# Kernel optimization log

Measured on AMD Instinct MI355X. Metric: run time of the kernel, lower is better.

## Reference

```python
import jax, jax.numpy as jnp
import numpy as np

N, FP, H, E, B = 60000, 120, 512, 3, 600
NNZ = 5_000_000
NFORCE = 3 * N
ELEMENTS = jnp.array([1, 8, 29], dtype=jnp.int32)  # unique_atoms (H, O, Cu)


def setup_inputs():
    key = jax.random.key(0)
    ks = jax.random.split(key, 10)
    fingerprints = jax.random.normal(ks[0], (N, FP), jnp.float32)
    atomic_numbers = ELEMENTS[jax.random.randint(ks[1], (N,), 0, E)]
    image_idx = jnp.sort(jax.random.randint(ks[2], (N,), 0, B)).astype(jnp.int32)
    W1 = jax.random.normal(ks[3], (E, FP, H), jnp.float32) / np.float32(np.sqrt(FP))
    b1 = jnp.zeros((E, H), jnp.float32)
    W2 = jax.random.normal(ks[4], (E, H, H), jnp.float32) / np.float32(np.sqrt(H))
    b2 = jnp.zeros((E, H), jnp.float32)
    W3 = jax.random.normal(ks[5], (E, H, 1), jnp.float32) / np.float32(np.sqrt(H))
    b3 = jnp.zeros((E, 1), jnp.float32)
    # sparse fprimes [N*FP, 3*N] in COO form
    fprime_rows = jax.random.randint(ks[6], (NNZ,), 0, N * FP).astype(jnp.int32)
    fprime_cols = jax.random.randint(ks[7], (NNZ,), 0, NFORCE).astype(jnp.int32)
    fprime_vals = jax.random.normal(ks[8], (NNZ,), jnp.float32) * 0.01
    return {"fingerprints": fingerprints, "atomic_numbers": atomic_numbers,
            "image_idx": image_idx, "W1": W1, "b1": b1, "W2": W2, "b2": b2,
            "W3": W3, "b3": b3, "fprime_rows": fprime_rows,
            "fprime_cols": fprime_cols, "fprime_vals": fprime_vals}


def _energy(fingerprints, W1, b1, W2, b2, W3, b3, mask, image_idx):
    # stacked per-element 3-layer tanh MLPs, evaluated densely over all atoms
    h = jnp.tanh(jnp.einsum('nf,efh->enh', fingerprints, W1) + b1[:, None, :])
    h = jnp.tanh(jnp.einsum('enh,ehk->enk', h, W2) + b2[:, None, :])
    out = jnp.einsum('enh,eho->eno', h, W3) + b3[:, None, :]  # [E, N, 1]
    o = jnp.sum(mask.T * out[..., 0], axis=0)  # mask-select per-atom energy [N]
    return jax.ops.segment_sum(o, image_idx, num_segments=B)  # per-image energy [B]


def reference(fingerprints, atomic_numbers, image_idx, W1, b1, W2, b2, W3, b3,
              fprime_rows, fprime_cols, fprime_vals):
    # ElementMask: one-hot over unique atomic numbers
    mask = (atomic_numbers[:, None] == ELEMENTS[None, :]).astype(fingerprints.dtype)  # [N, E]
    efn = lambda fp: _energy(fp, W1, b1, W2, b2, W3, b3, mask, image_idx)
    energy, vjp_fn = jax.vjp(efn, fingerprints)
    # grad of energy wrt fingerprints with grad_outputs = ones
    g = vjp_fn(jnp.ones_like(energy))[0].reshape(-1)  # [N*FP]
    # forces = -fprimes^T @ g  via sparse scatter
    forces = -jax.ops.segment_sum(fprime_vals * g[fprime_rows], fprime_cols,
                                  num_segments=NFORCE).reshape(-1, 3)  # [N, 3]
    return (energy, forces)
```

## Files before the change

kernel.cpp:

```cpp
#include <hip/hip_runtime.h>

#define N_ATOMS 60000
#define FPD 120
#define HD 512
#define EE 3
#define BB 600
#define NNZ_C 5000000
#define NFORCE (3 * N_ATOMS)
#define TB 32
#define CBITS 12
#define NBUCK ((NFORCE + 4095) / 4096)
#define NSLOT 16

typedef unsigned short ushort_t;
typedef unsigned int uint_t;
typedef unsigned long long u64_t;
typedef __attribute__((ext_vector_type(8))) __bf16 bf16x8;
typedef __attribute__((ext_vector_type(4))) float f32x4;
typedef __attribute__((ext_vector_type(4))) int i32x4;

union BF8 { f32x4 f; bf16x8 h; };

__device__ __forceinline__ ushort_t f2bf(float x) {
    uint_t u = __builtin_bit_cast(uint_t, x);
    u = (u + 0x7FFFu + ((u >> 16) & 1u)) >> 16;
    return (ushort_t)u;
}
__device__ __forceinline__ float bf2f(ushort_t s) {
    uint_t u = ((uint_t)s) << 16;
    return __builtin_bit_cast(float, u);
}
__device__ __forceinline__ float fast_tanh(float x) {
    float e2 = __expf(2.f * x);
    return fmaf(-2.f, __frcp_rn(e2 + 1.f), 1.f);
}

__global__ __launch_bounds__(256) void build_lists(const int* __restrict__ z,
                                                   int* __restrict__ counts,
                                                   int* __restrict__ lists) {
    __shared__ int lc[3];
    __shared__ int lbase[3];
    const int t = threadIdx.x;
    if (t < 3) lc[t] = 0;
    __syncthreads();
    const int i = blockIdx.x * 256 + t;
    int e = 0, pos = 0;
    if (i < N_ATOMS) {
        int zi = z[i];
        e = (zi == 1) ? 0 : ((zi == 8) ? 1 : 2);
        pos = atomicAdd(&lc[e], 1);
    }
    __syncthreads();
    if (t < 3) lbase[t] = atomicAdd(&counts[t], lc[t]);
    __syncthreads();
    if (i < N_ATOMS) lists[e * N_ATOMS + lbase[e] + pos] = i;
}

#define R_W2 (EE * 16 * 32 * 512)
#define R_W1 (EE * 4 * 32 * 512)
#define R_W1T (EE * 16 * 8 * 512)
__global__ __launch_bounds__(256) void pack_all(
    const float* __restrict__ W1, const float* __restrict__ W2,
    ushort_t* __restrict__ W1p, ushort_t* __restrict__ W2p,
    ushort_t* __restrict__ W2Tp, ushort_t* __restrict__ W1Tp) {
    int idx = blockIdx.x * 256 + threadIdx.x;
    if (idx < R_W2) {
        int p = idx;
        int j = p & 7, L = (p >> 3) & 63, ct = (p >> 9) & 31, ks = (p >> 14) & 15, e = p >> 18;
        int k = ks * 32 + ((L >> 4) << 3) + j;
        int n = (ct << 4) + (L & 15);
        W2p[p]  = f2bf(W2[((e << 9) + k) * 512 + n]);
        W2Tp[p] = f2bf(W2[((e << 9) + n) * 512 + k]);
    } else if (idx < R_W2 + R_W1) {
        int p = idx - R_W2;
        int j = p & 7, L = (p >> 3) & 63, ct = (p >> 9) & 31, ks = (p >> 14) & 3, e = p >> 16;
        int k = ks * 32 + ((L >> 4) << 3) + j;
        int n = (ct << 4) + (L & 15);
        W1p[p] = (k < FPD) ? f2bf(W1[(e * FPD + k) * 512 + n]) : (ushort_t)0;
    } else if (idx < R_W2 + R_W1 + R_W1T) {
        int p = idx - R_W2 - R_W1;
        int j = p & 7, L = (p >> 3) & 63, ct = (p >> 9) & 7, ks = (p >> 12) & 15, e = p >> 16;
        int k = ks * 32 + ((L >> 4) << 3) + j;
        int n = (ct << 4) + (L & 15);
        W1Tp[p] = (n < FPD) ? f2bf(W1[(e * FPD + n) * 512 + k]) : (ushort_t)0;
    }
}

#define STR 520
#define FSTR 136

__global__ __launch_bounds__(512, 4) void mlp_mfma(
    const float* __restrict__ fps, const int* __restrict__ image_idx,
    const float* __restrict__ b1, const float* __restrict__ b2,
    const float* __restrict__ W3, const float* __restrict__ b3,
    const ushort_t* __restrict__ W1p, const ushort_t* __restrict__ W2p,
    const ushort_t* __restrict__ W2Tp, const ushort_t* __restrict__ W1Tp,
    const int* __restrict__ counts, const int* __restrict__ lists,
    float* __restrict__ energy, ushort_t* __restrict__ g) {
    __shared__ ushort_t sH1[TB * STR];
    __shared__ ushort_t sD[TB * STR];
    __shared__ float sW3[512];
    __shared__ float eAcc[TB];
    __shared__ int sAtom[TB];
    __shared__ int sImg[TB];

    const int e = blockIdx.x % EE;
    const int tile = blockIdx.x / EE;
    const int cnt = counts[e];
    const int base = tile * TB;
    if (base >= cnt) return;
    const int nA = min(TB, cnt - base);
    const int* lst = lists + e * N_ATOMS + base;

    const int t = threadIdx.x;
    const int w = t >> 6, lane = t & 63, quad = lane >> 4, lc = lane & 15;

    if (t < TB) {
        int a = (t < nA) ? lst[t] : -1;
        sAtom[t] = a;
        sImg[t] = (a >= 0) ? image_idx[a] : 0;
        eAcc[t] = 0.f;
    }
    if (t < 512) sW3[t] = W3[e * 512 + t];
    for (int i = t; i < TB * 128; i += 512) {
        int a = i >> 7, f = i & 127;
        float v = 0.f;
        if (f < FPD && a < nA) v = __builtin_nontemporal_load(&fps[(long long)lst[a] * FPD + f]);
        sD[a * FSTR + f] = f2bf(v);
    }
    __syncthreads();

    float b1c[4], b2c[4];
#pragma unroll
    for (int c = 0; c < 4; c++) {
        int col = w * 64 + c * 16 + lc;
        b1c[c] = b1[e * 512 + col];
        b2c[c] = b2[e * 512 + col];
    }

    f32x4 acc[2][4];

#pragma unroll
    for (int rt = 0; rt < 2; rt++)
#pragma unroll
        for (int c = 0; c < 4; c++) acc[rt][c] = (f32x4)0.f;
    {
        const ushort_t* wbase = W1p + ((size_t)(e * 4) * 32 + w * 4) * 512 + lane * 8;
        BF8 bb[4][4];
#pragma unroll
        for (int ks = 0; ks < 4; ks++)
#pragma unroll
            for (int c = 0; c < 4; c++)
                bb[ks][c].f = *(const f32x4*)(wbase + ((size_t)ks * 32 + c) * 512);
#pragma unroll
        for (int ks = 0; ks < 4; ks++) {
            bf16x8 a0 = *(const bf16x8*)((const char*)sD + lc * (FSTR * 2) + ks * 64 + quad * 16);
            bf16x8 a1 = *(const bf16x8*)((const char*)sD + (16 + lc) * (FSTR * 2) + ks * 64 + quad * 16);
#pragma unroll
            for (int c = 0; c < 4; c++) {
                acc[0][c] = __builtin_amdgcn_mfma_f32_16x16x32_bf16(a0, bb[ks][c].h, acc[0][c], 0, 0, 0);
                acc[1][c] = __builtin_amdgcn_mfma_f32_16x16x32_bf16(a1, bb[ks][c].h, acc[1][c], 0, 0, 0);
            }
        }
    }
#pragma unroll
    for (int c = 0; c < 4; c++) {
        int col = w * 64 + c * 16 + lc;
#pragma unroll
        for (int rt = 0; rt < 2; rt++)
#pragma unroll
            for (int r = 0; r < 4; r++) {
                int row = rt * 16 + quad * 4 + r;
                sH1[row * STR + col] = f2bf(fast_tanh(acc[rt][c][r] + b1c[c]));
            }
    }
    __syncthreads();

#pragma unroll
    for (int rt = 0; rt < 2; rt++)
#pragma unroll
        for (int c = 0; c < 4; c++) acc[rt][c] = (f32x4)0.f;
    {
        const ushort_t* wbase = W2p + ((size_t)(e * 16) * 32 + w * 4) * 512 + lane * 8;
#pragma unroll
        for (int ksc = 0; ksc < 4; ksc++) {
            BF8 bb[4][4];
#pragma unroll
            for (int kk = 0; kk < 4; kk++)
#pragma unroll
                for (int c = 0; c < 4; c++)
                    bb[kk][c].f = *(const f32x4*)(wbase + (size_t)(ksc * 4 + kk) * 32 * 512 + (size_t)c * 512);
#pragma unroll
            for (int kk = 0; kk < 4; kk++) {
                int ks = ksc * 4 + kk;
                bf16x8 a0 = *(const bf16x8*)((const char*)sH1 + lc * (STR * 2) + ks * 64 + quad * 16);
                bf16x8 a1 = *(const bf16x8*)((const char*)sH1 + (16 + lc) * (STR * 2) + ks * 64 + quad * 16);
#pragma unroll
                for (int c = 0; c < 4; c++) {
                    acc[0][c] = __builtin_amdgcn_mfma_f32_16x16x32_bf16(a0, bb[kk][c].h, acc[0][c], 0, 0, 0);
                    acc[1][c] = __builtin_amdgcn_mfma_f32_16x16x32_bf16(a1, bb[kk][c].h, acc[1][c], 0, 0, 0);
                }
            }
        }
    }
    {
        float ep[2][4];
#pragma unroll
        for (int rt = 0; rt < 2; rt++)
#pragma unroll
            for (int r = 0; r < 4; r++) ep[rt][r] = 0.f;
#pragma unroll
        for (int c = 0; c < 4; c++) {
            int col = w * 64 + c * 16 + lc;
            float w3c = sW3[col];
#pragma unroll
            for (int rt = 0; rt < 2; rt++)
#pragma unroll
                for (int r = 0; r < 4; r++) {
                    int row = rt * 16 + quad * 4 + r;
                    float h2 = fast_tanh(acc[rt][c][r] + b2c[c]);
                    ep[rt][r] += h2 * w3c;
                    sD[row * STR + col] = f2bf(w3c * (1.f - h2 * h2));
                }
        }
#pragma unroll
        for (int rt = 0; rt < 2; rt++)
#pragma unroll
            for (int r = 0; r < 4; r++) {
                float p = ep[rt][r];
                p += __shfl_xor(p, 1);
                p += __shfl_xor(p, 2);
                p += __shfl_xor(p, 4);
                p += __shfl_xor(p, 8);
                if (lc == 0) atomicAdd(&eAcc[rt * 16 + quad * 4 + r], p);
            }
    }
    __syncthreads();

    if (t < nA) atomicAdd(&energy[sImg[t]], eAcc[t] + b3[e]);

#pragma unroll
    for (int rt = 0; rt < 2; rt++)
#pragma unroll
        for (int c = 0; c < 4; c++) acc[rt][c] = (f32x4)0.f;
    {
        const ushort_t* wbase = W2Tp + ((size_t)(e * 16) * 32 + w * 4) * 512 + lane * 8;
#pragma unroll
        for (int ksc = 0; ksc < 4; ksc++) {
            BF8 bb[4][4];
#pragma unroll
            for (int kk = 0; kk < 4; kk++)
#pragma unroll
                for (int c = 0; c < 4; c++)
                    bb[kk][c].f = *(const f32x4*)(wbase + (size_t)(ksc * 4 + kk) * 32 * 512 + (size_t)c * 512);
#pragma unroll
            for (int kk = 0; kk < 4; kk++) {
                int ks = ksc * 4 + kk;
                bf16x8 a0 = *(const bf16x8*)((const char*)sD + lc * (STR * 2) + ks * 64 + quad * 16);
                bf16x8 a1 = *(const bf16x8*)((const char*)sD + (16 + lc) * (STR * 2) + ks * 64 + quad * 16);
#pragma unroll
                for (int c = 0; c < 4; c++) {
                    acc[0][c] = __builtin_amdgcn_mfma_f32_16x16x32_bf16(a0, bb[kk][c].h, acc[0][c], 0, 0, 0);
                    acc[1][c] = __builtin_amdgcn_mfma_f32_16x16x32_bf16(a1, bb[kk][c].h, acc[1][c], 0, 0, 0);
                }
            }
        }
    }
#pragma unroll
    for (int c = 0; c < 4; c++) {
        int col = w * 64 + c * 16 + lc;
#pragma unroll
        for (int rt = 0; rt < 2; rt++)
#pragma unroll
            for (int r = 0; r < 4; r++) {
                int row = rt * 16 + quad * 4 + r;
                float h1v = bf2f(sH1[row * STR + col]);
                acc[rt][c][r] *= (1.f - h1v * h1v);
            }
    }
    __syncthreads();
#pragma unroll
    for (int c = 0; c < 4; c++) {
        int col = w * 64 + c * 16 + lc;
#pragma unroll
        for (int rt = 0; rt < 2; rt++)
#pragma unroll
            for (int r = 0; r < 4; r++) {
                int row = rt * 16 + quad * 4 + r;
                sH1[row * STR + col] = f2bf(acc[rt][c][r]);
            }
    }
    __syncthreads();

    f32x4 acc7[2];
#pragma unroll
    for (int rt = 0; rt < 2; rt++) acc7[rt] = (f32x4)0.f;
    {
        const ushort_t* wbase = W1Tp + ((size_t)(e * 16) * 8 + w) * 512 + lane * 8;
#pragma unroll
        for (int ksc = 0; ksc < 2; ksc++) {
            BF8 bb[8];
#pragma unroll
            for (int kk = 0; kk < 8; kk++)
                bb[kk].f = *(const f32x4*)(wbase + (size_t)(ksc * 8 + kk) * 8 * 512);
#pragma unroll
            for (int kk = 0; kk < 8; kk++) {
                int ks = ksc * 8 + kk;
                bf16x8 a0 = *(const bf16x8*)((const char*)sH1 + lc * (STR * 2) + ks * 64 + quad * 16);
                bf16x8 a1 = *(const bf16x8*)((const char*)sH1 + (16 + lc) * (STR * 2) + ks * 64 + quad * 16);
                acc7[0] = __builtin_amdgcn_mfma_f32_16x16x32_bf16(a0, bb[kk].h, acc7[0], 0, 0, 0);
                acc7[1] = __builtin_amdgcn_mfma_f32_16x16x32_bf16(a1, bb[kk].h, acc7[1], 0, 0, 0);
            }
        }
    }
    {
        int col = w * 16 + lc;
#pragma unroll
        for (int rt = 0; rt < 2; rt++)
#pragma unroll
            for (int r = 0; r < 4; r++) {
                int row = rt * 16 + quad * 4 + r;
                if (col < FPD && row < nA)
                    g[(long long)sAtom[row] * FPD + col] = f2bf(acc7[rt][r]);
            }
    }
}

__global__ __launch_bounds__(256) void bucket_hist(const int* __restrict__ cols,
                                                   int* __restrict__ bcnt) {
    __shared__ int h[NBUCK];
    const int t = threadIdx.x;
    if (t < NBUCK) h[t] = 0;
    __syncthreads();
    const int nv = NNZ_C / 4;
    for (int vk = blockIdx.x * 256 + t; vk < nv; vk += gridDim.x * 256) {
        i32x4 c = __builtin_nontemporal_load((const i32x4*)cols + vk);
        atomicAdd(&h[c.x >> CBITS], 1);
        atomicAdd(&h[c.y >> CBITS], 1);
        atomicAdd(&h[c.z >> CBITS], 1);
        atomicAdd(&h[c.w >> CBITS], 1);
    }
    __syncthreads();
    if (t < NBUCK) atomicAdd(&bcnt[t], h[t]);
}

__global__ void bucket_scan(const int* __restrict__ bcnt, int* __restrict__ bbase,
                            int* __restrict__ bcur) {
    if (threadIdx.x == 0 && blockIdx.x == 0) {
        int s = 0;
        for (int i = 0; i < NBUCK; i++) { bbase[i] = s; bcur[i] = s; s += bcnt[i]; }
    }
}

__global__ __launch_bounds__(256) void bucket_scatter(
    const int* __restrict__ rows, const int* __restrict__ cols,
    const float* __restrict__ vals, int* __restrict__ bcur,
    u64_t* __restrict__ bpack) {
    __shared__ int lcnt[NBUCK];
    __shared__ int lcur[NBUCK];
    const int t = threadIdx.x;
    if (t < NBUCK) lcnt[t] = 0;
    __syncthreads();
    const int vk0 = blockIdx.x * 2048;
    i32x4 ccache[8];
    int nb[8][4];
#pragma unroll
    for (int i = 0; i < 8; i++) {
        int vk = vk0 + i * 256 + t;
        if (vk * 4 < NNZ_C) {
            i32x4 c = __builtin_nontemporal_load((const i32x4*)cols + vk);
            ccache[i] = c;
            nb[i][0] = c.x >> CBITS; nb[i][1] = c.y >> CBITS;
            nb[i][2] = c.z >> CBITS; nb[i][3] = c.w >> CBITS;
            atomicAdd(&lcnt[nb[i][0]], 1);
            atomicAdd(&lcnt[nb[i][1]], 1);
            atomicAdd(&lcnt[nb[i][2]], 1);
            atomicAdd(&lcnt[nb[i][3]], 1);
        } else {
            nb[i][0] = -1;
        }
    }
    __syncthreads();
    if (t < NBUCK) lcur[t] = atomicAdd(&bcur[t], lcnt[t]);
    __syncthreads();
#pragma unroll
    for (int i = 0; i < 8; i++) {
        int vk = vk0 + i * 256 + t;
        if (vk * 4 < NNZ_C) {
            i32x4 r = __builtin_nontemporal_load((const i32x4*)rows + vk);
            f32x4 v = __builtin_nontemporal_load((const f32x4*)vals + vk);
            int rr[4] = {r.x, r.y, r.z, r.w};
            int cc[4] = {ccache[i].x, ccache[i].y, ccache[i].z, ccache[i].w};
            float vv[4] = {v.x, v.y, v.z, v.w};
#pragma unroll
            for (int u = 0; u < 4; u++) {
                int pos = atomicAdd(&lcur[nb[i][u]], 1);
                u64_t pk = (u64_t)(uint_t)rr[u] |
                           ((u64_t)(uint_t)(cc[u] & ((1 << CBITS) - 1)) << 23) |
                           ((u64_t)f2bf(vv[u]) << 35);
                bpack[pos] = pk;
            }
        }
    }
}

__global__ __launch_bounds__(256) void scatter_lds(
    const u64_t* __restrict__ bpack, const int* __restrict__ bbase,
    const int* __restrict__ bcnt, const ushort_t* __restrict__ g,
    float* __restrict__ forcesP) {
    __shared__ float facc[1 << CBITS];
    const int b = blockIdx.x >> 4;
    const int s = blockIdx.x & (NSLOT - 1);
    const int t = threadIdx.x;
    for (int i = t; i < (1 << CBITS); i += 256) facc[i] = 0.f;
    __syncthreads();
    const int base = bbase[b];
    const int end = base + bcnt[b];
    for (int i = base + s * 256 + t; i < end; i += NSLOT * 256) {
        u64_t pk = bpack[i];
        int r = (int)(pk & 0x7FFFFFu);
        int cin = (int)((pk >> 23) & 0xFFFu);
        float v = bf2f((ushort_t)(pk >> 35));
        atomicAdd(&facc[cin], -v * bf2f(g[r]));
    }
    __syncthreads();
    const int colbase = b << CBITS;
    float* fp = forcesP + (size_t)s * NFORCE;
    for (int i = t; i < (1 << CBITS); i += 256) {
        int col = colbase + i;
        if (col < NFORCE) __builtin_nontemporal_store(facc[i], &fp[col]);
    }
}

__global__ void reduce_forces(const float* __restrict__ forcesP, float* __restrict__ forces) {
    int i = blockIdx.x * blockDim.x + threadIdx.x;
    if (i >= NFORCE) return;
    float s = 0.f;
#pragma unroll
    for (int x = 0; x < NSLOT; x++) s += forcesP[(size_t)x * NFORCE + i];
    forces[i] = s;
}

__global__ __launch_bounds__(256) void scatter_forces(
    const int* __restrict__ rows, const int* __restrict__ cols,
    const float* __restrict__ vals, const ushort_t* __restrict__ g,
    float* __restrict__ forcesP) {
    int k = blockIdx.x * 256 + threadIdx.x;
    if (k >= NNZ_C / 4) return;
    int slot = blockIdx.x & (NSLOT - 1);
    i32x4 r = __builtin_nontemporal_load((const i32x4*)rows + k);
    i32x4 c = __builtin_nontemporal_load((const i32x4*)cols + k);
    f32x4 v = __builtin_nontemporal_load((const f32x4*)vals + k);
    float* fp = forcesP + (size_t)slot * NFORCE;
    atomicAdd(&fp[c.x], -v.x * bf2f(g[r.x]));
    atomicAdd(&fp[c.y], -v.y * bf2f(g[r.y]));
    atomicAdd(&fp[c.z], -v.z * bf2f(g[r.z]));
    atomicAdd(&fp[c.w], -v.w * bf2f(g[r.w]));
}

extern "C" void kernel_launch(void* const* d_in, const int* in_sizes, int n_in,
                              void* d_out, int out_size, void* d_ws, size_t ws_size,
                              hipStream_t stream) {
    const float* fps = (const float*)d_in[0];
    const int* z = (const int*)d_in[1];
    const int* img = (const int*)d_in[2];
    const float* W1 = (const float*)d_in[3];
    const float* b1 = (const float*)d_in[4];
    const float* W2 = (const float*)d_in[5];
    const float* b2 = (const float*)d_in[6];
    const float* W3 = (const float*)d_in[7];
    const float* b3 = (const float*)d_in[8];
    const int* rows = (const int*)d_in[9];
    const int* cols = (const int*)d_in[10];
    const float* vals = (const float*)d_in[11];

    float* out = (float*)d_out;
    float* energy = out;
    float* forces = out + BB;

    char* ws = (char*)d_ws;
    int* counts = (int*)ws;
    int* lists = (int*)(ws + 256);
    ushort_t* W1p = (ushort_t*)(ws + 720384);
    ushort_t* W2p = (ushort_t*)(ws + 1113600);
    ushort_t* W2Tp = (ushort_t*)(ws + 2686464);
    ushort_t* W1Tp = (ushort_t*)(ws + 4259328);
    ushort_t* g = (ushort_t*)(ws + 4652544);
    float* forcesP = (float*)(ws + 19052544);
    int* bmeta = (int*)(ws + 30572544);
    int* bcnt = bmeta, *bbase = bmeta + 64, *bcur = bmeta + 128;
    u64_t* bpack = (u64_t*)(ws + 30573568);
    const size_t WS_NEED = 70573568;
    (void)in_sizes; (void)n_in; (void)out_size;

    (void)hipMemsetAsync(energy, 0, BB * sizeof(float), stream);
    (void)hipMemsetAsync(counts, 0, 256, stream);

    build_lists<<<(N_ATOMS + 255) / 256, 256, 0, stream>>>(z, counts, lists);
    pack_all<<<(R_W2 + R_W1 + R_W1T + 255) / 256, 256, 0, stream>>>(
        W1, W2, W1p, W2p, W2Tp, W1Tp);

    int tiles = (N_ATOMS + TB - 1) / TB;
    mlp_mfma<<<EE * tiles, 512, 0, stream>>>(fps, img, b1, b2, W3, b3,
                                             W1p, W2p, W2Tp, W1Tp,
                                             counts, lists, energy, g);

    if (ws_size >= WS_NEED) {
        (void)hipMemsetAsync(bmeta, 0, 768, stream);
        bucket_hist<<<256, 256, 0, stream>>>(cols, bcnt);
        bucket_scan<<<1, 64, 0, stream>>>(bcnt, bbase, bcur);
        bucket_scatter<<<(NNZ_C + 8191) / 8192, 256, 0, stream>>>(
            rows, cols, vals, bcur, bpack);
        scatter_lds<<<NBUCK * NSLOT, 256, 0, stream>>>(bpack, bbase, bcnt, g, forcesP);
        reduce_forces<<<(NFORCE + 255) / 256, 256, 0, stream>>>(forcesP, forces);
    } else {
        (void)hipMemsetAsync(forcesP, 0, (size_t)NSLOT * NFORCE * sizeof(float), stream);
        scatter_forces<<<(NNZ_C / 4 + 255) / 256, 256, 0, stream>>>(rows, cols, vals, g, forcesP);
        reduce_forces<<<(NFORCE + 255) / 256, 256, 0, stream>>>(forcesP, forces);
    }
}
```

Measured before the change: 455.7 us.

## Shard LDS histograms, unroll bucket scatter loads, keep tanh activations in registers

Three separate changes. The layer-1 tanh outputs are now kept in fp32 registers and reused for the backward derivative, replacing a reload from LDS as bf16 (which also changes precision slightly). The bucket histogram and bucket scatter kernels split their LDS counters into four shards indexed by thread to reduce atomic contention; in the scatter kernel this makes each shard reserve its own range in every bucket. The LDS force accumulation loop is unrolled four times so the gathers of packed entries and g values can be in flight together, at the cost of more registers.

After: 521.7 us. 1.14x slower.

```diff
diff --git a/kernel.cpp b/kernel.cpp
--- a/kernel.cpp
+++ b/kernel.cpp
@@ -11,6 +11,7 @@
 #define CBITS 12
 #define NBUCK ((NFORCE + 4095) / 4096)
 #define NSLOT 16
+#define NSHARD 4
 
 typedef unsigned short ushort_t;
 typedef unsigned int uint_t;
@@ -139,6 +140,7 @@
     }
 
     f32x4 acc[2][4];
+    float h1f[2][4][4];
 
 #pragma unroll
     for (int rt = 0; rt < 2; rt++)
@@ -171,7 +173,9 @@
 #pragma unroll
             for (int r = 0; r < 4; r++) {
                 int row = rt * 16 + quad * 4 + r;
-                sH1[row * STR + col] = f2bf(fast_tanh(acc[rt][c][r] + b1c[c]));
+                float hv = fast_tanh(acc[rt][c][r] + b1c[c]);
+                h1f[rt][c][r] = hv;
+                sH1[row * STR + col] = f2bf(hv);
             }
     }
     __syncthreads();
@@ -267,17 +271,14 @@
         }
     }
 #pragma unroll
-    for (int c = 0; c < 4; c++) {
-        int col = w * 64 + c * 16 + lc;
+    for (int c = 0; c < 4; c++)
 #pragma unroll
         for (int rt = 0; rt < 2; rt++)
 #pragma unroll
             for (int r = 0; r < 4; r++) {
-                int row = rt * 16 + quad * 4 + r;
-                float h1v = bf2f(sH1[row * STR + col]);
-                acc[rt][c][r] *= (1.f - h1v * h1v);
-            }
-    }
+                float hv = h1f[rt][c][r];
+                acc[rt][c][r] *= (1.f - hv * hv);
+            }
     __syncthreads();
 #pragma unroll
     for (int c = 0; c < 4; c++) {
@@ -328,20 +329,26 @@
 
 __global__ __launch_bounds__(256) void bucket_hist(const int* __restrict__ cols,
                                                    int* __restrict__ bcnt) {
-    __shared__ int h[NBUCK];
+    __shared__ int h[NSHARD][NBUCK];
     const int t = threadIdx.x;
-    if (t < NBUCK) h[t] = 0;
-    __syncthreads();
+    if (t < NSHARD * NBUCK) h[t / NBUCK][t % NBUCK] = 0;
+    __syncthreads();
+    const int sh = t & (NSHARD - 1);
     const int nv = NNZ_C / 4;
     for (int vk = blockIdx.x * 256 + t; vk < nv; vk += gridDim.x * 256) {
         i32x4 c = __builtin_nontemporal_load((const i32x4*)cols + vk);
-        atomicAdd(&h[c.x >> CBITS], 1);
-        atomicAdd(&h[c.y >> CBITS], 1);
-        atomicAdd(&h[c.z >> CBITS], 1);
-        atomicAdd(&h[c.w >> CBITS], 1);
-    }
-    __syncthreads();
-    if (t < NBUCK) atomicAdd(&bcnt[t], h[t]);
+        atomicAdd(&h[sh][c.x >> CBITS], 1);
+        atomicAdd(&h[sh][c.y >> CBITS], 1);
+        atomicAdd(&h[sh][c.z >> CBITS], 1);
+        atomicAdd(&h[sh][c.w >> CBITS], 1);
+    }
+    __syncthreads();
+    if (t < NBUCK) {
+        int s = 0;
+#pragma unroll
+        for (int x = 0; x < NSHARD; x++) s += h[x][t];
+        atomicAdd(&bcnt[t], s);
+    }
 }
 
 __global__ void bucket_scan(const int* __restrict__ bcnt, int* __restrict__ bbase,
@@ -356,11 +363,12 @@
     const int* __restrict__ rows, const int* __restrict__ cols,
     const float* __restrict__ vals, int* __restrict__ bcur,
     u64_t* __restrict__ bpack) {
-    __shared__ int lcnt[NBUCK];
-    __shared__ int lcur[NBUCK];
+    __shared__ int lcnt[NSHARD][NBUCK];
+    __shared__ int lcur[NSHARD][NBUCK];
     const int t = threadIdx.x;
-    if (t < NBUCK) lcnt[t] = 0;
-    __syncthreads();
+    if (t < NSHARD * NBUCK) lcnt[t / NBUCK][t % NBUCK] = 0;
+    __syncthreads();
+    const int sh = t & (NSHARD - 1);
     const int vk0 = blockIdx.x * 2048;
     i32x4 ccache[8];
     int nb[8][4];
@@ -372,16 +380,19 @@
             ccache[i] = c;
             nb[i][0] = c.x >> CBITS; nb[i][1] = c.y >> CBITS;
             nb[i][2] = c.z >> CBITS; nb[i][3] = c.w >> CBITS;
-            atomicAdd(&lcnt[nb[i][0]], 1);
-            atomicAdd(&lcnt[nb[i][1]], 1);
-            atomicAdd(&lcnt[nb[i][2]], 1);
-            atomicAdd(&lcnt[nb[i][3]], 1);
+            atomicAdd(&lcnt[sh][nb[i][0]], 1);
+            atomicAdd(&lcnt[sh][nb[i][1]], 1);
+            atomicAdd(&lcnt[sh][nb[i][2]], 1);
+            atomicAdd(&lcnt[sh][nb[i][3]], 1);
         } else {
             nb[i][0] = -1;
         }
     }
     __syncthreads();
-    if (t < NBUCK) lcur[t] = atomicAdd(&bcur[t], lcnt[t]);
+    if (t < NSHARD * NBUCK) {
+        int x = t / NBUCK, b = t % NBUCK;
+        lcur[x][b] = atomicAdd(&bcur[b], lcnt[x][b]);
+    }
     __syncthreads();
 #pragma unroll
     for (int i = 0; i < 8; i++) {
@@ -394,7 +405,7 @@
             float vv[4] = {v.x, v.y, v.z, v.w};
 #pragma unroll
             for (int u = 0; u < 4; u++) {
-                int pos = atomicAdd(&lcur[nb[i][u]], 1);
+                int pos = atomicAdd(&lcur[sh][nb[i][u]], 1);
                 u64_t pk = (u64_t)(uint_t)rr[u] |
                            ((u64_t)(uint_t)(cc[u] & ((1 << CBITS) - 1)) << 23) |
                            ((u64_t)f2bf(vv[u]) << 35);
@@ -416,7 +427,23 @@
     __syncthreads();
     const int base = bbase[b];
     const int end = base + bcnt[b];
-    for (int i = base + s * 256 + t; i < end; i += NSLOT * 256) {
+    const int S = NSLOT * 256;
+    int i = base + s * 256 + t;
+    for (; i + 3 * S < end; i += 4 * S) {
+        u64_t p0 = bpack[i];
+        u64_t p1 = bpack[i + S];
+        u64_t p2 = bpack[i + 2 * S];
+        u64_t p3 = bpack[i + 3 * S];
+        float g0 = bf2f(g[(int)(p0 & 0x7FFFFFu)]);
+        float g1 = bf2f(g[(int)(p1 & 0x7FFFFFu)]);
+        float g2 = bf2f(g[(int)(p2 & 0x7FFFFFu)]);
+        float g3 = bf2f(g[(int)(p3 & 0x7FFFFFu)]);
+        atomicAdd(&facc[(int)((p0 >> 23) & 0xFFFu)], -bf2f((ushort_t)(p0 >> 35)) * g0);
+        atomicAdd(&facc[(int)((p1 >> 23) & 0xFFFu)], -bf2f((ushort_t)(p1 >> 35)) * g1);
+        atomicAdd(&facc[(int)((p2 >> 23) & 0xFFFu)], -bf2f((ushort_t)(p2 >> 35)) * g2);
+        atomicAdd(&facc[(int)((p3 >> 23) & 0xFFFu)], -bf2f((ushort_t)(p3 >> 35)) * g3);
+    }
+    for (; i < end; i += S) {
         u64_t pk = bpack[i];
         int r = (int)(pk & 0x7FFFFFu);
         int cin = (int)((pk >> 23) & 0xFFFu);
@@ -426,9 +453,9 @@
     __syncthreads();
     const int colbase = b << CBITS;
     float* fp = forcesP + (size_t)s * NFORCE;
-    for (int i = t; i < (1 << CBITS); i += 256) {
-        int col = colbase + i;
-        if (col < NFORCE) __builtin_nontemporal_store(facc[i], &fp[col]);
+    for (int j = t; j < (1 << CBITS); j += 256) {
+        int col = colbase + j;
+        if (col < NFORCE) __builtin_nontemporal_store(facc[j], &fp[col]);
     }
 }
 
```
